# Optimization experiments

Hardware: AMD Instinct MI355X
Metric: run time of the kernel (lower is better)

The kernel has to match this reference:

```python
import jax, jax.numpy as jnp
import numpy as np

EMBED_DIM = 1024
B, S = 4, 4096


def setup_inputs() -> dict:
    key = jax.random.key(0)
    kx, kq, kk, kv = jax.random.split(key, 4)
    x = jax.random.normal(kx, (B, S, EMBED_DIM), dtype=jnp.float32)
    W_Q = jax.random.normal(kq, (EMBED_DIM, EMBED_DIM), dtype=jnp.float32)
    W_K = jax.random.normal(kk, (EMBED_DIM, EMBED_DIM), dtype=jnp.float32)
    W_V = jax.random.normal(kv, (EMBED_DIM, EMBED_DIM), dtype=jnp.float32)
    return {"x": x, "W_Q": W_Q, "W_K": W_K, "W_V": W_V}


def reference(x, W_Q, W_K, W_V):
    # Q, K, V: [B, S, D]
    Q = x @ W_Q
    K = x @ W_K
    V = x @ W_V
    scale = 1.0 / jnp.sqrt(jnp.float32(EMBED_DIM))
    # scores: [B, S, S] (full score matrix, as in the original)
    scores = jnp.einsum('bsd,btd->bst', Q, K) * scale
    attn = jax.nn.softmax(scores, axis=-1)
    # output: [B, S, D]
    Z = jnp.einsum('bst,btd->bsd', attn, V)
    return Z
```

## Files before the change

kernel.cpp:

```cpp
#include <hip/hip_runtime.h>


typedef _Float16 half8 __attribute__((ext_vector_type(8)));
typedef _Float16 half4v __attribute__((ext_vector_type(4)));
typedef float floatx4 __attribute__((ext_vector_type(4)));

__device__ __forceinline__ void glds16(const _Float16* g, _Float16* l) {
    __builtin_amdgcn_global_load_lds(
        (const __attribute__((address_space(1))) void*)g,
        (__attribute__((address_space(3))) void*)l, 16, 0, 0);
}


__global__ __launch_bounds__(512, 2) void qk8(
    const _Float16* __restrict__ QH, const _Float16* __restrict__ QL,
    const _Float16* __restrict__ KH, const _Float16* __restrict__ KL,
    float* __restrict__ Sc, float* __restrict__ pmax, float scale)
{
    __shared__ _Float16 sP[2 * 32768];

    const int tid = threadIdx.x;
    const int bm = blockIdx.y, bn = blockIdx.x;
    const int lane = tid & 63, w = tid >> 6;
    const int quad = lane >> 4, lrow = lane & 15;
    const int wm = w >> 1, wn = w & 1;

    const int s0h = ((((lrow & 1) << 2) + quad) ^ ((lrow >> 1) & 7)) * 8;
    const int arow2 = wm * 32 + (lrow >> 1);
    const int brow2 = wn * 64 + (lrow >> 1);

    const int sp = (tid & 7) ^ ((tid >> 3) & 7);
    const int gR = 2 * (tid >> 3) + (sp >> 2);
    const int gk = (sp & 3) * 8;
    const size_t ga = (size_t)(bm * 256 + gR) * 1024 + gk;
    const size_t gb = (size_t)(bn * 256 + gR) * 1024 + gk;

    floatx4 acc[4][8] = {};

    auto stageAll = [&](int b, int ko) {
        _Float16* l = sP + b * 32768 + tid * 8;
        glds16(QH + ga + ko, l);
        glds16(QH + ga + ko + 131072, l + 4096);
        glds16(QL + ga + ko, l + 8192);
        glds16(QL + ga + ko + 131072, l + 12288);
        glds16(KH + gb + ko, l + 16384);
        glds16(KH + gb + ko + 131072, l + 20480);
        glds16(KL + gb + ko, l + 24576);
        glds16(KL + gb + ko + 131072, l + 28672);
    };

    stageAll(0, 0);

    #pragma unroll 1
    for (int c = 0; c < 32; ++c) {
        __syncthreads();

        if (c < 31) stageAll((c + 1) & 1, (c + 1) * 32);

        const int cb = (c & 1) * 32768;
        half8 aH[4], aL[4];
        #pragma unroll
        for (int mi = 0; mi < 4; ++mi) {
            aH[mi] = *(const half8*)&sP[cb + (arow2 + mi * 8) * 64 + s0h];
            aL[mi] = *(const half8*)&sP[cb + 8192 + (arow2 + mi * 8) * 64 + s0h];
        }
        #pragma unroll
        for (int q = 0; q < 4; ++q) {
            half8 bh[2], bl[2];
            #pragma unroll
            for (int nj = 0; nj < 2; ++nj) {
                bh[nj] = *(const half8*)&sP[cb + 16384 + (brow2 + q * 16 + nj * 8) * 64 + s0h];
                bl[nj] = *(const half8*)&sP[cb + 24576 + (brow2 + q * 16 + nj * 8) * 64 + s0h];
            }
            __builtin_amdgcn_s_setprio(1);
            #pragma unroll
            for (int mi = 0; mi < 4; ++mi)
                #pragma unroll
                for (int nj = 0; nj < 2; ++nj) {
                    acc[mi][q * 2 + nj] = __builtin_amdgcn_mfma_f32_16x16x32_f16(
                        aH[mi], bh[nj], acc[mi][q * 2 + nj], 0, 0, 0);
                    acc[mi][q * 2 + nj] = __builtin_amdgcn_mfma_f32_16x16x32_f16(
                        aH[mi], bl[nj], acc[mi][q * 2 + nj], 0, 0, 0);
                    acc[mi][q * 2 + nj] = __builtin_amdgcn_mfma_f32_16x16x32_f16(
                        aL[mi], bh[nj], acc[mi][q * 2 + nj], 0, 0, 0);
                }
            __builtin_amdgcn_s_setprio(0);
        }
    }

    asm volatile("s_waitcnt vmcnt(0) lgkmcnt(0)" ::: "memory");

    #pragma unroll
    for (int mi = 0; mi < 4; ++mi) {
        #pragma unroll
        for (int r = 0; r < 4; ++r) {
            const int grow = bm * 256 + wm * 64 + mi * 16 + quad * 4 + r;
            float v[8];
            #pragma unroll
            for (int nc = 0; nc < 8; ++nc) v[nc] = acc[mi][nc][r] * scale;
            float mx = fmaxf(fmaxf(fmaxf(v[0], v[1]), fmaxf(v[2], v[3])),
                             fmaxf(fmaxf(v[4], v[5]), fmaxf(v[6], v[7])));
            #pragma unroll
            for (int off = 1; off < 16; off <<= 1)
                mx = fmaxf(mx, __shfl_xor(mx, off));
            if (lrow == 0) pmax[(size_t)grow * 32 + bn * 2 + wn] = mx;
            float* so = Sc + (size_t)grow * 4096 + bn * 256 + wn * 128;
            #pragma unroll
            for (int nc = 0; nc < 8; ++nc) so[nc * 16 + lrow] = v[nc];
        }
    }
}

template <bool SPLITIN, int OMODE, bool PMAX>
__global__ __launch_bounds__(256, 2) void gemm_nt(
    const _Float16* AH, const _Float16* AL,
    const _Float16* BH, const _Float16* BL,
    void* out0, void* out1,
    const float* __restrict__ rdiv, float* __restrict__ pmax,
    float scale, int M, int N, int K, int Kst, int koff,
    const _Float16* BH2, const _Float16* BL2, void* o0b, void* o1b)
{
    if (blockIdx.z == 1) {
        BH = BH2; BL = BL2; out0 = o0b; out1 = o1b;
        AH += koff;
        if (SPLITIN) AL += koff;
    }

    __shared__ _Float16 sAH[2 * 128 * 32];
    __shared__ _Float16 sBH[2 * 128 * 32];
    __shared__ _Float16 sAL[SPLITIN ? 2 * 128 * 32 : 8];
    __shared__ _Float16 sBL[SPLITIN ? 2 * 128 * 32 : 8];

    const int tid = threadIdx.x;
    const int bm = blockIdx.y, bn = blockIdx.x;
    const int lane = tid & 63, quad = lane >> 4, lrow = lane & 15;
    const int wave = tid >> 6, wm = wave >> 1, wn = wave & 1;

    const int wb = (tid & 192) * 8;
    const size_t g0 = (size_t)(tid >> 2) * Kst + (tid & 3) * 8;
    const size_t g1 = (size_t)((256 + tid) >> 2) * Kst + (tid & 3) * 8;
    const _Float16* pA0 = AH + (size_t)bm * 128 * Kst + g0;
    const _Float16* pA1 = AH + (size_t)bm * 128 * Kst + g1;
    const _Float16* pB0 = BH + (size_t)bn * 128 * Kst + g0;
    const _Float16* pB1 = BH + (size_t)bn * 128 * Kst + g1;
    const _Float16* pA0L = SPLITIN ? (AL + (size_t)bm * 128 * Kst + g0) : nullptr;
    const _Float16* pA1L = SPLITIN ? (AL + (size_t)bm * 128 * Kst + g1) : nullptr;
    const _Float16* pB0L = SPLITIN ? (BL + (size_t)bn * 128 * Kst + g0) : nullptr;
    const _Float16* pB1L = SPLITIN ? (BL + (size_t)bn * 128 * Kst + g1) : nullptr;

    floatx4 acc[4][4] = {};

    const int aoff = (wm * 64 + lrow) * 32 + quad * 8;
    const int boff = (wn * 64 + lrow) * 32 + quad * 8;

    glds16(pA0, sAH + wb);        glds16(pA1, sAH + 2048 + wb);
    glds16(pB0, sBH + wb);        glds16(pB1, sBH + 2048 + wb);
    if (SPLITIN) {
        glds16(pA0L, sAL + wb);   glds16(pA1L, sAL + 2048 + wb);
        glds16(pB0L, sBL + wb);   glds16(pB1L, sBL + 2048 + wb);
    }
    pA0 += 32; pA1 += 32; pB0 += 32; pB1 += 32;
    if (SPLITIN) { pA0L += 32; pA1L += 32; pB0L += 32; pB1L += 32; }

    int cur = 0;
    for (int k0 = 0; k0 < K; k0 += 32) {
        __syncthreads();

        if (k0 + 32 < K) {
            const int nb = (cur ^ 1) * 4096;
            glds16(pA0, sAH + nb + wb);        glds16(pA1, sAH + nb + 2048 + wb);
            glds16(pB0, sBH + nb + wb);        glds16(pB1, sBH + nb + 2048 + wb);
            if (SPLITIN) {
                glds16(pA0L, sAL + nb + wb);   glds16(pA1L, sAL + nb + 2048 + wb);
                glds16(pB0L, sBL + nb + wb);   glds16(pB1L, sBL + nb + 2048 + wb);
            }
            pA0 += 32; pA1 += 32; pB0 += 32; pB1 += 32;
            if (SPLITIN) { pA0L += 32; pA1L += 32; pB0L += 32; pB1L += 32; }
        }

        const int cb = cur * 4096;
        half8 aH[4], bH[4], aL[4], bL[4];
        #pragma unroll
        for (int i = 0; i < 4; ++i) {
            aH[i] = *(const half8*)&sAH[cb + aoff + i * 16 * 32];
            bH[i] = *(const half8*)&sBH[cb + boff + i * 16 * 32];
            if (SPLITIN) {
                aL[i] = *(const half8*)&sAL[cb + aoff + i * 16 * 32];
                bL[i] = *(const half8*)&sBL[cb + boff + i * 16 * 32];
            }
        }
        #pragma unroll
        for (int mi = 0; mi < 4; ++mi)
            #pragma unroll
            for (int nj = 0; nj < 4; ++nj) {
                acc[mi][nj] = __builtin_amdgcn_mfma_f32_16x16x32_f16(
                    aH[mi], bH[nj], acc[mi][nj], 0, 0, 0);
                if (SPLITIN) {
                    acc[mi][nj] = __builtin_amdgcn_mfma_f32_16x16x32_f16(
                        aH[mi], bL[nj], acc[mi][nj], 0, 0, 0);
                    acc[mi][nj] = __builtin_amdgcn_mfma_f32_16x16x32_f16(
                        aL[mi], bH[nj], acc[mi][nj], 0, 0, 0);
                }
            }
        cur ^= 1;
    }

    #pragma unroll
    for (int mi = 0; mi < 4; ++mi) {
        #pragma unroll
        for (int r = 0; r < 4; ++r) {
            const int grow = bm * 128 + wm * 64 + mi * 16 + quad * 4 + r;
            float s = scale;
            if (OMODE == 1) s = scale / rdiv[grow];
            float v[4];
            #pragma unroll
            for (int nj = 0; nj < 4; ++nj) v[nj] = acc[mi][nj][r] * s;
            if (PMAX) {
                float mx = fmaxf(fmaxf(v[0], v[1]), fmaxf(v[2], v[3]));
                #pragma unroll
                for (int off = 1; off < 16; off <<= 1)
                    mx = fmaxf(mx, __shfl_xor(mx, off));
                if (lrow == 0) pmax[(size_t)grow * 64 + bn * 2 + wn] = mx;
            }
            #pragma unroll
            for (int nj = 0; nj < 4; ++nj) {
                const int gcol = bn * 128 + wn * 64 + nj * 16 + lrow;
                const size_t idx = (size_t)grow * N + gcol;
                if (OMODE <= 1) {
                    ((float*)out0)[idx] = v[nj];
                } else if (OMODE == 2) {
                    ((_Float16*)out0)[idx] = (_Float16)v[nj];
                } else {
                    const _Float16 h = (_Float16)v[nj];
                    ((_Float16*)out0)[idx] = h;
                    ((_Float16*)out1)[idx] = (_Float16)(v[nj] - (float)h);
                }
            }
        }
    }
}

__global__ __launch_bounds__(256) void pv_fin(
    const float* __restrict__ p, const float* __restrict__ rowsum,
    float* __restrict__ out, float scale, int n)
{
    int i = (blockIdx.x * 256 + threadIdx.x) * 4;
    const int stride = gridDim.x * 256 * 4;
    for (; i < n; i += stride) {
        float4 a = *(const float4*)(p + i);
        float4 b = *(const float4*)(p + i + n);
        const float r = scale / rowsum[i >> 10];
        float4 o;
        o.x = (a.x + b.x) * r; o.y = (a.y + b.y) * r;
        o.z = (a.z + b.z) * r; o.w = (a.w + b.w) * r;
        *(float4*)(out + i) = o;
    }
}

__global__ __launch_bounds__(256) void split_scale(
    const float* __restrict__ x, _Float16* __restrict__ hi,
    _Float16* __restrict__ lo, int n)
{
    int i = (blockIdx.x * 256 + threadIdx.x) * 4;
    const int stride = gridDim.x * 256 * 4;
    for (; i < n; i += stride) {
        float4 v = *(const float4*)(x + i);
        float a[4] = {v.x * 256.f, v.y * 256.f, v.z * 256.f, v.w * 256.f};
        half4v h, l;
        #pragma unroll
        for (int j = 0; j < 4; ++j) {
            h[j] = (_Float16)a[j];
            l[j] = (_Float16)(a[j] - (float)h[j]);
        }
        *(half4v*)(hi + i) = h;
        *(half4v*)(lo + i) = l;
    }
}

__global__ __launch_bounds__(256) void wprep3(
    const float* __restrict__ W0, const float* __restrict__ W1,
    const float* __restrict__ W2,
    _Float16* __restrict__ h0, _Float16* __restrict__ l0,
    _Float16* __restrict__ h1, _Float16* __restrict__ l1,
    _Float16* __restrict__ h2, int dim)
{
    const int z = blockIdx.z;
    const float* W = (z == 0) ? W0 : (z == 1) ? W1 : W2;
    _Float16* hiT = (z == 0) ? h0 : (z == 1) ? h1 : h2;
    _Float16* loT = (z == 0) ? l0 : (z == 1) ? l1 : nullptr;

    __shared__ float t[32][33];
    const int n0 = blockIdx.x * 32, k0 = blockIdx.y * 32;
    const int tx = threadIdx.x, ty = threadIdx.y;
    #pragma unroll
    for (int i = 0; i < 4; ++i)
        t[ty + 8 * i][tx] = 256.f * W[(size_t)(k0 + ty + 8 * i) * dim + n0 + tx];
    __syncthreads();
    #pragma unroll
    for (int i = 0; i < 4; ++i) {
        const int nn = ty + 8 * i;
        const float v = t[tx][nn];
        const _Float16 h = (_Float16)v;
        const size_t o = (size_t)(n0 + nn) * dim + k0 + tx;
        hiT[o] = h;
        if (loT) loT[o] = (_Float16)(v - (float)h);
    }
}

__global__ __launch_bounds__(256) void softmax_p(
    const float* __restrict__ Sc, const float* __restrict__ pmax,
    _Float16* __restrict__ P, float* __restrict__ rowsum)
{
    __shared__ float red[8];
    const int tid = threadIdx.x;
    const int row = blockIdx.x;
    const float* srow = Sc + (size_t)row * 4096;
    _Float16* prow = P + (size_t)row * 4096;

    if (tid < 32) {
        float m = pmax[(size_t)row * 32 + tid];
        #pragma unroll
        for (int off = 16; off; off >>= 1) m = fmaxf(m, __shfl_xor(m, off));
        if (tid == 0) red[0] = m;
    }
    __syncthreads();
    const float rmax = red[0];

    float s = 0.f;
    for (int c = tid * 4; c < 4096; c += 1024) {
        float4 v = *(const float4*)(srow + c);
        float p0 = __expf(v.x - rmax), p1 = __expf(v.y - rmax);
        float p2 = __expf(v.z - rmax), p3 = __expf(v.w - rmax);
        s += p0 + p1 + p2 + p3;
        half4v h = {(_Float16)p0, (_Float16)p1, (_Float16)p2, (_Float16)p3};
        *(half4v*)(prow + c) = h;
    }
    #pragma unroll
    for (int off = 32; off; off >>= 1) s += __shfl_xor(s, off, 64);
    if ((tid & 63) == 0) red[4 + (tid >> 6)] = s;
    __syncthreads();
    if (tid == 0) rowsum[row] = red[4] + red[5] + red[6] + red[7];
}

extern "C" void kernel_launch(void* const* d_in, const int* in_sizes, int n_in,
                              void* d_out, int out_size, void* d_ws, size_t ws_size,
                              hipStream_t stream) {
    const int Bb = 4, S = 4096, D = 1024;
    const size_t SD = (size_t)S * D;
    const size_t SS = (size_t)S * S;

    const float* x  = (const float*)d_in[0];
    const float* WQ = (const float*)d_in[1];
    const float* WK = (const float*)d_in[2];
    const float* WV = (const float*)d_in[3];
    float* out = (float*)d_out;

    char* w = (char*)d_ws;
    _Float16* WQhT = (_Float16*)w;  w += (size_t)D * D * 2;
    _Float16* WQlT = (_Float16*)w;  w += (size_t)D * D * 2;
    _Float16* WKhT = (_Float16*)w;  w += (size_t)D * D * 2;
    _Float16* WKlT = (_Float16*)w;  w += (size_t)D * D * 2;
    _Float16* WvhT = (_Float16*)w;  w += (size_t)D * D * 2;
    _Float16* xhi  = (_Float16*)w;  w += SD * 2;
    _Float16* xlo  = (_Float16*)w;  w += SD * 2;
    _Float16* Qhi  = (_Float16*)w;  w += SD * 2;
    _Float16* Qlo  = (_Float16*)w;  w += SD * 2;
    _Float16* Khi  = (_Float16*)w;  w += SD * 2;
    _Float16* Klo  = (_Float16*)w;  w += SD * 2;
    _Float16* VT   = (_Float16*)w;  w += SD * 2;
    float*    rowsum = (float*)w;   w += (size_t)S * 4;
    float*    pmax = (float*)w;     w += (size_t)S * 64 * 4;
    float*    Sc   = (float*)w;     w += SS * 4;
    _Float16* P    = (_Float16*)w;  w += SS * 2;
    float*    pvp  = (float*)w;     w += SD * 2 * 4;

    const float kInv256 = 0.00390625f;
    const float kScScale = 4.76837158203125e-7f;

    dim3 blk(256);

    wprep3<<<dim3(32, 32, 3), dim3(32, 8), 0, stream>>>(
        WQ, WK, WV, WQhT, WQlT, WKhT, WKlT, WvhT, D);

    for (int b = 0; b < Bb; ++b) {
        const float* xb = x + (size_t)b * SD;
        float* outb = out + (size_t)b * SD;

        split_scale<<<dim3(4096), blk, 0, stream>>>(xb, xhi, xlo, (int)SD);

        gemm_nt<true, 3, false><<<dim3(D / 128, S / 128, 2), blk, 0, stream>>>(
            xhi, xlo, WQhT, WQlT, Qhi, Qlo, nullptr, nullptr, kInv256, S, D,
            D, D, 0, WKhT, WKlT, Khi, Klo);

        gemm_nt<false, 2, false><<<dim3(S / 128, D / 128, 1), blk, 0, stream>>>(
            WvhT, nullptr, xhi, nullptr, VT, nullptr, nullptr, nullptr, kInv256,
            D, S, D, D, 0, nullptr, nullptr, nullptr, nullptr);

        qk8<<<dim3(S / 256, S / 256), dim3(512), 0, stream>>>(
            Qhi, Qlo, Khi, Klo, Sc, pmax, kScScale);

        softmax_p<<<dim3(S), blk, 0, stream>>>(Sc, pmax, P, rowsum);

        gemm_nt<false, 0, false><<<dim3(D / 128, S / 128, 2), blk, 0, stream>>>(
            P, nullptr, VT, nullptr, pvp, nullptr, nullptr, nullptr, 1.0f,
            S, D, S / 2, S, S / 2,
            VT + S / 2, nullptr, (void*)(pvp + SD), nullptr);

        pv_fin<<<dim3(2048), blk, 0, stream>>>(pvp, rowsum, outb, kInv256, (int)SD);
    }
}
```

Before: 1.074 ms.

## Shrink QK tile to 256x128, drop double buffering, raise occupancy to 4 blocks

The QK score kernel now computes a 256x128 tile instead of 256x256. It uses a single-buffered LDS stage of 48KB instead of 128KB and half the accumulator registers, and its launch bounds allow 4 blocks per CU. The aim is to hide load latency through higher occupancy instead of explicit double buffering. The trade-off is an extra barrier per K step with no in-block load/compute overlap, twice as many Q-tile reloads from memory, and twice as many partial-max entries (64 per row) for softmax to reduce.

```diff
diff --git a/kernel.cpp b/kernel.cpp
--- a/kernel.cpp
+++ b/kernel.cpp
@@ -12,12 +12,12 @@
 }
 
 
-__global__ __launch_bounds__(512, 2) void qk8(
+__global__ __launch_bounds__(512, 4) void qk8(
     const _Float16* __restrict__ QH, const _Float16* __restrict__ QL,
     const _Float16* __restrict__ KH, const _Float16* __restrict__ KL,
     float* __restrict__ Sc, float* __restrict__ pmax, float scale)
 {
-    __shared__ _Float16 sP[2 * 32768];
+    __shared__ _Float16 sP[24576];
 
     const int tid = threadIdx.x;
     const int bm = blockIdx.y, bn = blockIdx.x;
@@ -27,63 +27,52 @@
 
     const int s0h = ((((lrow & 1) << 2) + quad) ^ ((lrow >> 1) & 7)) * 8;
     const int arow2 = wm * 32 + (lrow >> 1);
-    const int brow2 = wn * 64 + (lrow >> 1);
+    const int brow2 = wn * 32 + (lrow >> 1);
 
     const int sp = (tid & 7) ^ ((tid >> 3) & 7);
     const int gR = 2 * (tid >> 3) + (sp >> 2);
     const int gk = (sp & 3) * 8;
     const size_t ga = (size_t)(bm * 256 + gR) * 1024 + gk;
-    const size_t gb = (size_t)(bn * 256 + gR) * 1024 + gk;
-
-    floatx4 acc[4][8] = {};
-
-    auto stageAll = [&](int b, int ko) {
-        _Float16* l = sP + b * 32768 + tid * 8;
+    const size_t gb = (size_t)(bn * 128 + gR) * 1024 + gk;
+
+    floatx4 acc[4][4] = {};
+
+    auto stageAll = [&](int ko) {
+        _Float16* l = sP + tid * 8;
         glds16(QH + ga + ko, l);
         glds16(QH + ga + ko + 131072, l + 4096);
         glds16(QL + ga + ko, l + 8192);
         glds16(QL + ga + ko + 131072, l + 12288);
         glds16(KH + gb + ko, l + 16384);
-        glds16(KH + gb + ko + 131072, l + 20480);
-        glds16(KL + gb + ko, l + 24576);
-        glds16(KL + gb + ko + 131072, l + 28672);
+        glds16(KL + gb + ko, l + 20480);
     };
-
-    stageAll(0, 0);
 
     #pragma unroll 1
     for (int c = 0; c < 32; ++c) {
+        if (c) __syncthreads();
+        stageAll(c * 32);
         __syncthreads();
 
-        if (c < 31) stageAll((c + 1) & 1, (c + 1) * 32);
-
-        const int cb = (c & 1) * 32768;
         half8 aH[4], aL[4];
         #pragma unroll
         for (int mi = 0; mi < 4; ++mi) {
-            aH[mi] = *(const half8*)&sP[cb + (arow2 + mi * 8) * 64 + s0h];
-            aL[mi] = *(const half8*)&sP[cb + 8192 + (arow2 + mi * 8) * 64 + s0h];
-        }
-        #pragma unroll
-        for (int q = 0; q < 4; ++q) {
-            half8 bh[2], bl[2];
-            #pragma unroll
-            for (int nj = 0; nj < 2; ++nj) {
-                bh[nj] = *(const half8*)&sP[cb + 16384 + (brow2 + q * 16 + nj * 8) * 64 + s0h];
-                bl[nj] = *(const half8*)&sP[cb + 24576 + (brow2 + q * 16 + nj * 8) * 64 + s0h];
-            }
+            aH[mi] = *(const half8*)&sP[(arow2 + mi * 8) * 64 + s0h];
+            aL[mi] = *(const half8*)&sP[8192 + (arow2 + mi * 8) * 64 + s0h];
+        }
+        #pragma unroll
+        for (int nc = 0; nc < 4; ++nc) {
+            half8 bh = *(const half8*)&sP[16384 + (brow2 + nc * 8) * 64 + s0h];
+            half8 bl = *(const half8*)&sP[20480 + (brow2 + nc * 8) * 64 + s0h];
             __builtin_amdgcn_s_setprio(1);
             #pragma unroll
-            for (int mi = 0; mi < 4; ++mi)
-                #pragma unroll
-                for (int nj = 0; nj < 2; ++nj) {
-                    acc[mi][q * 2 + nj] = __builtin_amdgcn_mfma_f32_16x16x32_f16(
-                        aH[mi], bh[nj], acc[mi][q * 2 + nj], 0, 0, 0);
-                    acc[mi][q * 2 + nj] = __builtin_amdgcn_mfma_f32_16x16x32_f16(
-                        aH[mi], bl[nj], acc[mi][q * 2 + nj], 0, 0, 0);
-                    acc[mi][q * 2 + nj] = __builtin_amdgcn_mfma_f32_16x16x32_f16(
-                        aL[mi], bh[nj], acc[mi][q * 2 + nj], 0, 0, 0);
-                }
+            for (int mi = 0; mi < 4; ++mi) {
+                acc[mi][nc] = __builtin_amdgcn_mfma_f32_16x16x32_f16(
+                    aH[mi], bh, acc[mi][nc], 0, 0, 0);
+                acc[mi][nc] = __builtin_amdgcn_mfma_f32_16x16x32_f16(
+                    aH[mi], bl, acc[mi][nc], 0, 0, 0);
+                acc[mi][nc] = __builtin_amdgcn_mfma_f32_16x16x32_f16(
+                    aL[mi], bh, acc[mi][nc], 0, 0, 0);
+            }
             __builtin_amdgcn_s_setprio(0);
         }
     }
@@ -95,18 +84,17 @@
         #pragma unroll
         for (int r = 0; r < 4; ++r) {
             const int grow = bm * 256 + wm * 64 + mi * 16 + quad * 4 + r;
-            float v[8];
-            #pragma unroll
-            for (int nc = 0; nc < 8; ++nc) v[nc] = acc[mi][nc][r] * scale;
-            float mx = fmaxf(fmaxf(fmaxf(v[0], v[1]), fmaxf(v[2], v[3])),
-                             fmaxf(fmaxf(v[4], v[5]), fmaxf(v[6], v[7])));
+            float v[4];
+            #pragma unroll
+            for (int nc = 0; nc < 4; ++nc) v[nc] = acc[mi][nc][r] * scale;
+            float mx = fmaxf(fmaxf(v[0], v[1]), fmaxf(v[2], v[3]));
             #pragma unroll
             for (int off = 1; off < 16; off <<= 1)
                 mx = fmaxf(mx, __shfl_xor(mx, off));
-            if (lrow == 0) pmax[(size_t)grow * 32 + bn * 2 + wn] = mx;
-            float* so = Sc + (size_t)grow * 4096 + bn * 256 + wn * 128;
-            #pragma unroll
-            for (int nc = 0; nc < 8; ++nc) so[nc * 16 + lrow] = v[nc];
+            if (lrow == 0) pmax[(size_t)grow * 64 + bn * 2 + wn] = mx;
+            float* so = Sc + (size_t)grow * 4096 + bn * 128 + wn * 64;
+            #pragma unroll
+            for (int nc = 0; nc < 4; ++nc) so[nc * 16 + lrow] = v[nc];
         }
     }
 }
@@ -317,10 +305,10 @@
     const float* srow = Sc + (size_t)row * 4096;
     _Float16* prow = P + (size_t)row * 4096;
 
-    if (tid < 32) {
-        float m = pmax[(size_t)row * 32 + tid];
-        #pragma unroll
-        for (int off = 16; off; off >>= 1) m = fmaxf(m, __shfl_xor(m, off));
+    if (tid < 64) {
+        float m = pmax[(size_t)row * 64 + tid];
+        #pragma unroll
+        for (int off = 32; off; off >>= 1) m = fmaxf(m, __shfl_xor(m, off));
         if (tid == 0) red[0] = m;
     }
     __syncthreads();
@@ -396,7 +384,7 @@
             WvhT, nullptr, xhi, nullptr, VT, nullptr, nullptr, nullptr, kInv256,
             D, S, D, D, 0, nullptr, nullptr, nullptr, nullptr);
 
-        qk8<<<dim3(S / 256, S / 256), dim3(512), 0, stream>>>(
+        qk8<<<dim3(S / 128, S / 256), dim3(512), 0, stream>>>(
             Qhi, Qlo, Khi, Klo, Sc, pmax, kScScale);
 
         softmax_p<<<dim3(S), blk, 0, stream>>>(Sc, pmax, P, rowsum);
```

After: 1.099 ms. +2.3%, slower.
